# Optimization experiments

Hardware: AMD Instinct MI355X
Metric: run time of the kernel (lower is better)

## Reference

```python
import jax, jax.numpy as jnp
import numpy as np


def _bilinear_align_corners(img, H, W):
    """Bilinear resize of img [B,K,h,w] to [B,K,H,W], align_corners=True."""
    h, w = img.shape[-2], img.shape[-1]
    ys = jnp.linspace(0.0, h - 1.0, H)
    xs = jnp.linspace(0.0, w - 1.0, W)
    y0 = jnp.clip(jnp.floor(ys).astype(jnp.int32), 0, h - 1)
    y1 = jnp.minimum(y0 + 1, h - 1)
    x0 = jnp.clip(jnp.floor(xs).astype(jnp.int32), 0, w - 1)
    x1 = jnp.minimum(x0 + 1, w - 1)
    wy = (ys - y0.astype(img.dtype))[:, None]   # [H,1]
    wx = (xs - x0.astype(img.dtype))            # [W]
    r0 = img[:, :, y0, :]                        # [B,K,H,w]
    r1 = img[:, :, y1, :]
    top = r0[..., x0] * (1.0 - wx) + r0[..., x1] * wx   # [B,K,H,W]
    bot = r1[..., x0] * (1.0 - wx) + r1[..., x1] * wx
    return top * (1.0 - wy) + bot * wy


def setup_inputs() -> dict:
    key = jax.random.key(0)
    k1, k2, k3 = jax.random.split(key, 3)
    B, C, h, w = 8, 256, 64, 64
    H, W = 512, 512
    K = 21
    feature_map = jax.random.normal(k1, (B, C, h, w), dtype=jnp.float32)
    x = jax.random.uniform(k2, (B, 3, H, W), dtype=jnp.float32)
    W_cls = jax.random.normal(k3, (K, C), dtype=jnp.float32) * 0.02
    b_cls = jnp.zeros((K,), dtype=jnp.float32)
    return {"feature_map": feature_map, "x": x, "W_cls": W_cls, "b_cls": b_cls}


def reference(feature_map, x, W_cls, b_cls):
    # 1x1 conv == channel contraction
    logits = jnp.einsum('bchw,kc->bkhw', feature_map, W_cls) + b_cls[None, :, None, None]
    seg = jax.nn.softmax(logits, axis=1)                      # [B,K,h,w]
    H, W = x.shape[2], x.shape[3]
    seg = _bilinear_align_corners(seg, H, W)                  # [B,K,H,W]
    xi = jnp.transpose(x, (0, 2, 3, 1))                       # [B,H,W,3]
    # q[b,k,c] = mean over (H,W) of x * seg_k  (the per-class loop, fused)
    q = jnp.einsum('bhwc,bkhw->bkc', xi, seg) / (H * W)       # [B,K,3]
    # attn[b,k,h,w] = sum_c x[b,h,w,c] * q[b,k,c]
    segments_by_color = jnp.einsum('bhwc,bkc->bkhw', xi, q)   # [B,K,H,W]
    return segments_by_color
```

## Files before the change

kernel.cpp:

```cpp
#include <hip/hip_runtime.h>
#include <math.h>

#define NB 8
#define NC 256
#define HS 64
#define WSM 64
#define HL 512
#define WL 512
#define NK 21
#define PS (HS*WSM)
#define PL (HL*WL)

#define NROWS (NB*3*HL)
#define WT_ELEMS (NK*NC)
#define WT_BLOCKS ((WT_ELEMS+63)/64)

typedef float fx4 __attribute__((ext_vector_type(4)));


__global__ __launch_bounds__(64) void k_prep(
    const float* __restrict__ x, const float* __restrict__ Wc,
    float* __restrict__ T1, float* __restrict__ Wt, float* __restrict__ q)
{
    int blk = blockIdx.x;
    int tid = threadIdx.x;

    if (blk < NROWS) {
        __shared__ float row[WL];
        const fx4* src4 = (const fx4*)(x + (size_t)blk * WL);
        fx4* row4 = (fx4*)row;
        row4[tid]      = src4[tid];
        row4[tid + 64] = src4[tid + 64];
        __syncthreads();

        const int w = tid;
        const float scale = 63.0f / 511.0f;
        const float inv_scale = 511.0f / 63.0f;
        int Xlo = max(0,    (int)floorf((w - 1) * inv_scale) - 1);
        int Xhi = min(WL-1, (int)ceilf ((w + 1) * inv_scale) + 1);
        float acc = 0.f;
        for (int X = Xlo; X <= Xhi; ++X) {
            float fs = X * scale;
            int i0 = (int)fs; if (i0 > WSM-1) i0 = WSM-1;
            float f = fs - (float)i0;
            int i1 = min(i0 + 1, WSM-1);
            float wt = (i0 == w ? 1.f - f : 0.f) + (i1 == w ? f : 0.f);
            acc += wt * row[X];
        }
        T1[(size_t)blk * WSM + w] = acc;
    } else if (blk < NROWS + WT_BLOCKS) {
        int i = (blk - NROWS) * 64 + tid;
        if (i < WT_ELEMS) {
            int c = i / NK;
            int k = i - c*NK;
            Wt[c*32 + k] = Wc[k*NC + c];
        }
    } else {
        for (int i = tid; i < NB*NK*3; i += 64) q[i] = 0.f;
    }
}

__global__ __launch_bounds__(256) void k_fused(
    const float* __restrict__ fm, const float* __restrict__ Wt,
    const float* __restrict__ bc, const float* __restrict__ T1,
    float* __restrict__ q)
{
    int b = blockIdx.y;
    int lane = threadIdx.x & 63;
    int wv   = threadIdx.x >> 6;
    int h    = blockIdx.x;
    int p = h * 64 + lane;

    __shared__ float sA[3][64];
    __shared__ float red[4][NK][64];

    if (wv < 3) {
        const float scale = 63.0f / 511.0f;
        const float inv_scale = 511.0f / 63.0f;
        int Ylo = max(0,    (int)floorf((h - 1) * inv_scale) - 1);
        int Yhi = min(HL-1, (int)ceilf ((h + 1) * inv_scale) + 1);
        const float* src = T1 + (size_t)(b*3 + wv) * HL * WSM + lane;
        float acc = 0.f;
        for (int Y = Ylo; Y <= Yhi; ++Y) {
            float fs = Y * scale;
            int i0 = (int)fs; if (i0 > HS-1) i0 = HS-1;
            float f = fs - (float)i0;
            int i1 = min(i0 + 1, HS-1);
            float wt = (i0 == h ? 1.f - f : 0.f) + (i1 == h ? f : 0.f);
            acc += wt * src[(size_t)Y * WSM];
        }
        sA[wv][lane] = acc;
    }

    float part[NK];
    #pragma unroll
    for (int k = 0; k < NK; ++k) part[k] = 0.f;

    const float* fmb = fm + (size_t)b * NC * PS + (size_t)(wv * 64) * PS + p;
    #pragma unroll 8
    for (int cc = 0; cc < 64; ++cc) {
        float v = __builtin_nontemporal_load(fmb + (size_t)cc * PS);
        const float* w = Wt + (wv * 64 + cc) * 32;
        #pragma unroll
        for (int k = 0; k < NK; ++k) part[k] = fmaf(v, w[k], part[k]);
    }

    #pragma unroll
    for (int k = 0; k < NK; ++k) red[wv][k][lane] = part[k];
    __syncthreads();

    float logit[NK];
    #pragma unroll
    for (int k = 0; k < NK; ++k)
        logit[k] = bc[k] + ((red[0][k][lane] + red[1][k][lane])
                          + (red[2][k][lane] + red[3][k][lane]));

    float m = logit[0];
    #pragma unroll
    for (int k = 1; k < NK; ++k) m = fmaxf(m, logit[k]);
    float s = 0.f;
    #pragma unroll
    for (int k = 0; k < NK; ++k) { logit[k] = __expf(logit[k] - m); s += logit[k]; }
    float inv = 1.f / s;

    float a0 = sA[0][lane], a1 = sA[1][lane], a2 = sA[2][lane];

    float* qb = q + b * NK * 3;
    for (int k = wv; k < NK; k += 4) {
        float sv = logit[k] * inv;
        float r0 = sv * a0, r1 = sv * a1, r2 = sv * a2;
        #pragma unroll
        for (int off = 32; off; off >>= 1) {
            r0 += __shfl_down(r0, off);
            r1 += __shfl_down(r1, off);
            r2 += __shfl_down(r2, off);
        }
        if (lane == 0) {
            atomicAdd(qb + k*3 + 0, r0);
            atomicAdd(qb + k*3 + 1, r1);
            atomicAdd(qb + k*3 + 2, r2);
        }
    }
}

__global__ __launch_bounds__(256) void k_out(
    const float* __restrict__ x, const float* __restrict__ q,
    float* __restrict__ out)
{
    __shared__ float sq[NK*3];
    int tid = threadIdx.x;
    int b = blockIdx.y;
    if (tid < NK*3) sq[tid] = q[b*NK*3 + tid] * (1.0f / (float)PL);
    __syncthreads();

    int p4 = blockIdx.x * 256 + tid;
    const fx4* xb = (const fx4*)(x + (size_t)b * 3 * PL);
    fx4 x0 = xb[p4];
    fx4 x1 = xb[PL/4 + p4];
    fx4 x2 = xb[2*(PL/4) + p4];
    fx4* ob = (fx4*)(out + (size_t)b * NK * PL);
    #pragma unroll
    for (int k = 0; k < NK; ++k) {
        fx4 o = sq[k*3+0]*x0 + sq[k*3+1]*x1 + sq[k*3+2]*x2;
        __builtin_nontemporal_store(o, ob + (size_t)k * (PL/4) + p4);
    }
}

extern "C" void kernel_launch(void* const* d_in, const int* in_sizes, int n_in,
                              void* d_out, int out_size, void* d_ws, size_t ws_size,
                              hipStream_t stream)
{
    const float* fm = (const float*)d_in[0];
    const float* x  = (const float*)d_in[1];
    const float* Wc = (const float*)d_in[2];
    const float* bc = (const float*)d_in[3];
    float* out = (float*)d_out;

    float* ws = (float*)d_ws;
    float* Wt = ws;
    float* T1 = Wt + 8192;
    float* q  = T1 + 786432;

    k_prep<<<NROWS + WT_BLOCKS + 1, 64, 0, stream>>>(x, Wc, T1, Wt, q);
    k_fused<<<dim3(HS, NB), 256, 0, stream>>>(fm, Wt, bc, T1, q);
    k_out<<<dim3(PL/4/256, NB), 256, 0, stream>>>(x, q, out);
}
```

Before: 279.9 us.

## Fuse separable bilinear-transpose reduction of x into fused logits kernel

Removes the row-wise prep pass over x that wrote an intermediate T1 buffer, and instead performs both vertical and horizontal weighted reductions of x inside the fused kernel using shared memory. This eliminates thousands of tiny prep blocks and the T1 write/read round trip. Block indices are swizzled so neighboring blocks span different batches. The fused kernel now does more serial work per block before its main channel loop, which may lengthen its critical path.

```diff
diff --git a/kernel.cpp b/kernel.cpp
--- a/kernel.cpp
+++ b/kernel.cpp
@@ -11,7 +11,6 @@
 #define PS (HS*WSM)
 #define PL (HL*WL)
 
-#define NROWS (NB*3*HL)
 #define WT_ELEMS (NK*NC)
 #define WT_BLOCKS ((WT_ELEMS+63)/64)
 
@@ -19,37 +18,12 @@
 
 
 __global__ __launch_bounds__(64) void k_prep(
-    const float* __restrict__ x, const float* __restrict__ Wc,
-    float* __restrict__ T1, float* __restrict__ Wt, float* __restrict__ q)
+    const float* __restrict__ Wc, float* __restrict__ Wt, float* __restrict__ q)
 {
     int blk = blockIdx.x;
     int tid = threadIdx.x;
-
-    if (blk < NROWS) {
-        __shared__ float row[WL];
-        const fx4* src4 = (const fx4*)(x + (size_t)blk * WL);
-        fx4* row4 = (fx4*)row;
-        row4[tid]      = src4[tid];
-        row4[tid + 64] = src4[tid + 64];
-        __syncthreads();
-
-        const int w = tid;
-        const float scale = 63.0f / 511.0f;
-        const float inv_scale = 511.0f / 63.0f;
-        int Xlo = max(0,    (int)floorf((w - 1) * inv_scale) - 1);
-        int Xhi = min(WL-1, (int)ceilf ((w + 1) * inv_scale) + 1);
-        float acc = 0.f;
-        for (int X = Xlo; X <= Xhi; ++X) {
-            float fs = X * scale;
-            int i0 = (int)fs; if (i0 > WSM-1) i0 = WSM-1;
-            float f = fs - (float)i0;
-            int i1 = min(i0 + 1, WSM-1);
-            float wt = (i0 == w ? 1.f - f : 0.f) + (i1 == w ? f : 0.f);
-            acc += wt * row[X];
-        }
-        T1[(size_t)blk * WSM + w] = acc;
-    } else if (blk < NROWS + WT_BLOCKS) {
-        int i = (blk - NROWS) * 64 + tid;
+    if (blk < WT_BLOCKS) {
+        int i = blk * 64 + tid;
         if (i < WT_ELEMS) {
             int c = i / NK;
             int k = i - c*NK;
@@ -62,34 +36,55 @@
 
 __global__ __launch_bounds__(256) void k_fused(
     const float* __restrict__ fm, const float* __restrict__ Wt,
-    const float* __restrict__ bc, const float* __restrict__ T1,
+    const float* __restrict__ bc, const float* __restrict__ x,
     float* __restrict__ q)
 {
-    int b = blockIdx.y;
+    int id = blockIdx.x;
+    int swz = (id & 7) * 64 + (id >> 3);
+    int b = swz >> 6;
+    int h = swz & 63;
     int lane = threadIdx.x & 63;
     int wv   = threadIdx.x >> 6;
-    int h    = blockIdx.x;
     int p = h * 64 + lane;
 
+    __shared__ float tmp[3][WL];
     __shared__ float sA[3][64];
     __shared__ float red[4][NK][64];
 
+    const float scale = 63.0f / 511.0f;
+    const float inv_scale = 511.0f / 63.0f;
+
     if (wv < 3) {
-        const float scale = 63.0f / 511.0f;
-        const float inv_scale = 511.0f / 63.0f;
         int Ylo = max(0,    (int)floorf((h - 1) * inv_scale) - 1);
         int Yhi = min(HL-1, (int)ceilf ((h + 1) * inv_scale) + 1);
-        const float* src = T1 + (size_t)(b*3 + wv) * HL * WSM + lane;
-        float acc = 0.f;
+        const float* xc = x + (size_t)(b*3 + wv) * PL;
+        fx4 acc0 = {0.f,0.f,0.f,0.f}, acc1 = {0.f,0.f,0.f,0.f};
         for (int Y = Ylo; Y <= Yhi; ++Y) {
             float fs = Y * scale;
             int i0 = (int)fs; if (i0 > HS-1) i0 = HS-1;
             float f = fs - (float)i0;
             int i1 = min(i0 + 1, HS-1);
             float wt = (i0 == h ? 1.f - f : 0.f) + (i1 == h ? f : 0.f);
-            acc += wt * src[(size_t)Y * WSM];
+            const fx4* xr = (const fx4*)(xc + (size_t)Y * WL);
+            acc0 += wt * xr[lane];
+            acc1 += wt * xr[lane + 64];
         }
-        sA[wv][lane] = acc;
+        fx4* t4 = (fx4*)tmp[wv];
+        t4[lane]      = acc0;
+        t4[lane + 64] = acc1;
+        const int w_ = lane;
+        int Xlo = max(0,    (int)floorf((w_ - 1) * inv_scale) - 1);
+        int Xhi = min(WL-1, (int)ceilf ((w_ + 1) * inv_scale) + 1);
+        float a = 0.f;
+        for (int X = Xlo; X <= Xhi; ++X) {
+            float fs = X * scale;
+            int i0 = (int)fs; if (i0 > WSM-1) i0 = WSM-1;
+            float f = fs - (float)i0;
+            int i1 = min(i0 + 1, WSM-1);
+            float wt = (i0 == w_ ? 1.f - f : 0.f) + (i1 == w_ ? f : 0.f);
+            a = fmaf(wt, tmp[wv][X], a);
+        }
+        sA[wv][lane] = a;
     }
 
     float part[NK];
@@ -178,10 +173,9 @@
 
     float* ws = (float*)d_ws;
     float* Wt = ws;
-    float* T1 = Wt + 8192;
-    float* q  = T1 + 786432;
+    float* q  = Wt + 8192;
 
-    k_prep<<<NROWS + WT_BLOCKS + 1, 64, 0, stream>>>(x, Wc, T1, Wt, q);
-    k_fused<<<dim3(HS, NB), 256, 0, stream>>>(fm, Wt, bc, T1, q);
+    k_prep<<<WT_BLOCKS + 1, 64, 0, stream>>>(Wc, Wt, q);
+    k_fused<<<NB*HS, 256, 0, stream>>>(fm, Wt, bc, x, q);
     k_out<<<dim3(PL/4/256, NB), 256, 0, stream>>>(x, q, out);
 }
```

Result: faster. 268.8 us (-4.0%).
